# Kernel tuning notes

Measured on AMD Instinct MI355X. Metric: run time of the kernel, lower is better.

## Reference

```python
import jax, jax.numpy as jnp
import numpy as np

EPS = 1e-5


def setup_inputs() -> dict:
    key = jax.random.key(0)
    ks = jax.random.split(key, 10)
    B, C, H, W = 8, 128, 64, 64
    inputs = jax.random.normal(ks[0], (B, C, H, W), dtype=jnp.float32)
    # GroupNorm affine params
    gn_w = jnp.ones((C,), dtype=jnp.float32)
    gn_b = jnp.zeros((C,), dtype=jnp.float32)
    # Linear layers: torch nn.Linear weight is [out, in]
    s = 1.0 / np.sqrt(C)
    Wq = jax.random.uniform(ks[1], (C, C), jnp.float32, -s, s)
    bq = jax.random.uniform(ks[2], (C,), jnp.float32, -s, s)
    Wk = jax.random.uniform(ks[3], (C, C), jnp.float32, -s, s)
    bk = jax.random.uniform(ks[4], (C,), jnp.float32, -s, s)
    Wv = jax.random.uniform(ks[5], (C, C), jnp.float32, -s, s)
    bv = jax.random.uniform(ks[6], (C,), jnp.float32, -s, s)
    Wp = jax.random.uniform(ks[7], (C, C), jnp.float32, -s, s)
    bp = jax.random.uniform(ks[8], (C,), jnp.float32, -s, s)
    return {"inputs": inputs, "gn_w": gn_w, "gn_b": gn_b,
            "Wq": Wq, "bq": bq, "Wk": Wk, "bk": bk,
            "Wv": Wv, "bv": bv, "Wp": Wp, "bp": bp,
            "groups": 32}


def _group_norm(x, w, b, groups):
    B, C, H, W = x.shape
    xg = x.reshape(B, groups, C // groups, H, W)
    mu = jnp.mean(xg, axis=(2, 3, 4), keepdims=True)
    var = jnp.var(xg, axis=(2, 3, 4), keepdims=True)
    xn = ((xg - mu) * jax.lax.rsqrt(var + EPS)).reshape(B, C, H, W)
    return xn * w[None, :, None, None] + b[None, :, None, None]


def reference(inputs, gn_w, gn_b, Wq, bq, Wk, bk, Wv, bv, Wp, bp, groups):
    B, C, H, W = inputs.shape
    scale = C ** (-0.5)
    normed = _group_norm(inputs, gn_w, gn_b, groups)  # [B,C,H,W]
    x = normed.transpose(0, 2, 3, 1).reshape(B, H * W, C)  # [B,N,C] tokens
    q = x @ Wq.T + bq
    k = x @ Wk.T + bk
    v = x @ Wv.T + bv
    # full dense attention over N = H*W tokens, single head
    scores = jnp.einsum('bnc,bmc->bnm', q, k) * scale  # [B,N,N]
    attn = jax.nn.softmax(scores, axis=-1)
    out = jnp.einsum('bnm,bmc->bnc', attn, v)
    proj = out @ Wp.T + bp
    proj = proj.reshape(B, H, W, C).transpose(0, 3, 1, 2)
    return normed + proj
```

## Files before the change

### kernel.cpp

```cpp
#include <hip/hip_runtime.h>
#include <hip/hip_bf16.h>
#include <math.h>

typedef __bf16 bf16_t;
typedef __bf16 bf16x8 __attribute__((ext_vector_type(8)));
typedef float  f32x4  __attribute__((ext_vector_type(4)));
typedef float  f32x16 __attribute__((ext_vector_type(16)));

#define BB 8
#define CC 128
#define NN 4096
#define LDP 136
#define SCALE2 0.12751743342f

static __device__ __forceinline__ f32x4 mfma16(bf16x8 a, bf16x8 b, f32x4 c) {
    return __builtin_amdgcn_mfma_f32_16x16x32_bf16(a, b, c, 0, 0, 0);
}
static __device__ __forceinline__ f32x16 mfma32(bf16x8 a, bf16x8 b, f32x16 c) {
    return __builtin_amdgcn_mfma_f32_32x32x16_bf16(a, b, c, 0, 0, 0);
}
static __device__ __forceinline__ void gld16(const void* g, void* l) {
    __builtin_amdgcn_global_load_lds(
        (const __attribute__((address_space(1))) void*)g,
        (__attribute__((address_space(3))) void*)l, 16, 0, 0);
}
static __device__ __forceinline__ unsigned pack2bf(float a, float b) {
    union { bf16_t h[2]; unsigned u; } r;
    r.h[0] = (bf16_t)a; r.h[1] = (bf16_t)b;
    return r.u;
}

__global__ void __launch_bounds__(256) gn_stats(const float* __restrict__ in,
                                                float* __restrict__ stats) {
    int bg = blockIdx.x;
    const float4* p4 = (const float4*)(in + (size_t)bg * 16384);
    int tid = threadIdx.x;
    float s = 0.f, ss = 0.f;
    for (int i = tid; i < 4096; i += 256) {
        float4 v = p4[i];
        s  += v.x + v.y + v.z + v.w;
        ss += v.x*v.x + v.y*v.y + v.z*v.z + v.w*v.w;
    }
    for (int off = 1; off < 64; off <<= 1) {
        s  += __shfl_xor(s,  off, 64);
        ss += __shfl_xor(ss, off, 64);
    }
    __shared__ float red[8];
    int wv = tid >> 6;
    if ((tid & 63) == 0) { red[wv*2] = s; red[wv*2+1] = ss; }
    __syncthreads();
    if (tid == 0) {
        float S  = red[0]+red[2]+red[4]+red[6];
        float SS = red[1]+red[3]+red[5]+red[7];
        float mu  = S * (1.f/16384.f);
        float var = SS * (1.f/16384.f) - mu*mu;
        stats[bg*2]   = mu;
        stats[bg*2+1] = rsqrtf(var + 1e-5f);
    }
}

__global__ void __launch_bounds__(256) gn_apply(const float* __restrict__ in,
                                                const float* __restrict__ gw,
                                                const float* __restrict__ gb,
                                                const float* __restrict__ stats,
                                                bf16_t* __restrict__ x) {
    int b  = blockIdx.x >> 6;
    int p0 = (blockIdx.x & 63) << 6;
    int tid = threadIdx.x;
    __shared__ bf16_t tile[64 * 130];
    for (int i = tid; i < 8192; i += 256) {
        int c = i >> 6, p = i & 63;
        size_t idx = ((size_t)(b*CC + c)) * NN + p0 + p;
        float v = in[idx];
        int sg = b*32 + (c >> 2);
        float xn = (v - stats[sg*2]) * stats[sg*2+1] * gw[c] + gb[c];
        tile[p*130 + c] = (bf16_t)xn;
    }
    __syncthreads();
    bf16_t* xb = x + ((size_t)(b*NN + p0)) * CC;
    for (int i = tid; i < 4096; i += 256) {
        int p = i >> 6, cp = i & 63;
        unsigned int d = *(const unsigned int*)&tile[p*130 + cp*2];
        *(unsigned int*)&xb[p*CC + cp*2] = d;
    }
}

__global__ void __launch_bounds__(256) qkv_gemm(const bf16_t* __restrict__ x,
        const float* __restrict__ Wq, const float* __restrict__ bq,
        const float* __restrict__ Wk, const float* __restrict__ bk,
        const float* __restrict__ Wv, const float* __restrict__ bv,
        bf16_t* __restrict__ q, bf16_t* __restrict__ k, bf16_t* __restrict__ vT) {
    __shared__ bf16_t wb[CC * LDP];
    const int ph  = blockIdx.x >> 8;
    const int blk = blockIdx.x & 255;
    int b  = blk >> 5;
    int n0 = (blk & 31) << 7;
    int tid = threadIdx.x;
    int lane = tid & 63, l15 = lane & 15, quad = lane >> 4;
    int w = tid >> 6;
    bf16x8 afr[2][4];
    #pragma unroll
    for (int rt = 0; rt < 2; rt++)
        #pragma unroll
        for (int kb = 0; kb < 4; kb++)
            afr[rt][kb] = *(const bf16x8*)&x[(size_t)(b*NN + n0 + w*32 + rt*16 + l15)*CC + kb*32 + quad*8];

    const float* W  = (ph == 0) ? Wq : (ph == 1 ? Wk : Wv);
    const float* bs = (ph == 0) ? bq : (ph == 1 ? bk : bv);
    for (int i = tid; i < 2048; i += 256) {
        int row = i >> 4, s8 = i & 15;
        const float* wp = W + row*128 + s8*8;
        bf16x8 v;
        #pragma unroll
        for (int j = 0; j < 8; j++) v[j] = (bf16_t)wp[j];
        *(bf16x8*)&wb[row*LDP + s8*8] = v;
    }
    __syncthreads();
    f32x4 acc[2][8];
    f32x4 z = {0.f, 0.f, 0.f, 0.f};
    #pragma unroll
    for (int rt = 0; rt < 2; rt++)
        #pragma unroll
        for (int t = 0; t < 8; t++) acc[rt][t] = z;
    #pragma unroll
    for (int kb = 0; kb < 4; kb++)
        #pragma unroll
        for (int t = 0; t < 8; t++) {
            bf16x8 bf = *(const bf16x8*)&wb[(t*16 + l15)*LDP + kb*32 + quad*8];
            acc[0][t] = mfma16(afr[0][kb], bf, acc[0][t]);
            acc[1][t] = mfma16(afr[1][kb], bf, acc[1][t]);
        }
    __syncthreads();
    if (ph < 2) {
        float sc = (ph == 0) ? SCALE2 : 1.0f;
        #pragma unroll
        for (int t = 0; t < 8; t++) {
            float bias = bs[t*16 + l15];
            #pragma unroll
            for (int rt = 0; rt < 2; rt++)
                #pragma unroll
                for (int r = 0; r < 4; r++) {
                    int nloc = w*32 + rt*16 + quad*4 + r;
                    wb[nloc*LDP + t*16 + l15] = (bf16_t)((acc[rt][t][r] + bias) * sc);
                }
        }
        __syncthreads();
        bf16_t* outp = (ph == 0) ? q : k;
        for (int i = tid; i < 2048; i += 256) {
            int row = i >> 4, g = i & 15;
            bf16x8 vv = *(const bf16x8*)&wb[row*LDP + g*8];
            int gd = (ph == 0) ? g : (g ^ (row & 15));
            *(bf16x8*)&outp[(size_t)(b*NN + n0 + row)*CC + gd*8] = vv;
        }
    } else {
        #pragma unroll
        for (int t = 0; t < 8; t++) {
            float bias = bs[t*16 + l15];
            #pragma unroll
            for (int rt = 0; rt < 2; rt++)
                #pragma unroll
                for (int r = 0; r < 4; r++) {
                    int nloc = w*32 + rt*16 + quad*4 + r;
                    wb[(t*16 + l15)*LDP + nloc] = (bf16_t)(acc[rt][t][r] + bias);
                }
        }
        __syncthreads();
        for (int i = tid; i < 8192; i += 256) {
            int c = i >> 6, np = i & 63;
            unsigned int d = *(const unsigned int*)&wb[c*LDP + np*2];
            int npp = (np & ~6) | ((np & 2) << 1) | ((np & 4) >> 1);
            int g = (npp >> 2) ^ (c & 15);
            *(unsigned int*)&vT[(size_t)(b*CC + c)*NN + n0 + (g << 3) + ((npp & 3) << 1)] = d;
        }
    }
}

__global__ void __launch_bounds__(512, 2) flash_attn(const bf16_t* __restrict__ qg_,
                                                     const bf16_t* __restrict__ kg,
                                                     const bf16_t* __restrict__ vg,
                                                     unsigned* __restrict__ opd,
                                                     float* __restrict__ mlf) {
    __shared__ bf16_t kbuf[2][128*128];
    __shared__ bf16_t vbuf[2][128*128];
    const int b    = blockIdx.x >> 5;
    const int qb   = (blockIdx.x >> 1) & 15;
    const int jh   = blockIdx.x & 1;
    const int q0   = qb << 8;
    const int j00  = jh << 11;
    const int tid  = threadIdx.x;
    const int lane = tid & 63;
    const int l31  = lane & 31;
    const int h    = lane >> 5;
    const int w    = tid >> 6;

    bf16x8 qf[8];
    {
        const bf16_t* qr = qg_ + ((size_t)(b*NN + q0 + w*32 + l31))*CC + h*8;
        #pragma unroll
        for (int kc = 0; kc < 8; kc++) qf[kc] = *(const bf16x8*)(qr + kc*16);
    }
    int gofs[8];
    #pragma unroll
    for (int kc = 0; kc < 8; kc++) gofs[kc] = ((2*kc + h) ^ (l31 & 15)) << 3;

    f32x16 ot[4];
    #pragma unroll
    for (int ct = 0; ct < 4; ct++)
        #pragma unroll
        for (int r = 0; r < 16; r++) ot[ct][r] = 0.f;
    float l = 0.f;

    {
        const bf16_t* kt = kg + ((size_t)(b*NN + j00))*CC;
        #pragma unroll
        for (int it = 0; it < 4; it++) {
            int cb = it*512 + tid;
            gld16(kt + (size_t)cb*8, &kbuf[0][cb*8]);
        }
        #pragma unroll
        for (int it = 0; it < 4; it++) {
            int c = it*512 + tid;
            gld16(vg + ((size_t)(b*CC + (c >> 4)))*NN + j00 + (c & 15)*8, &vbuf[0][c*8]);
        }
    }
    __syncthreads();

    for (int i = 0; i < 16; i++) {
        const int cur = i & 1;
        if (i < 15) {
            const int j0n = j00 + ((i + 1) << 7);
            const bf16_t* kt = kg + ((size_t)(b*NN + j0n))*CC;
            #pragma unroll
            for (int it = 0; it < 4; it++) {
                int cb = it*512 + tid;
                gld16(kt + (size_t)cb*8, &kbuf[cur^1][cb*8]);
            }
            #pragma unroll
            for (int it = 0; it < 4; it++) {
                int c = it*512 + tid;
                gld16(vg + ((size_t)(b*CC + (c >> 4)))*NN + j0n + (c & 15)*8, &vbuf[cur^1][c*8]);
            }
        }
        f32x16 st[4];
        #pragma unroll
        for (int tt = 0; tt < 4; tt++)
            #pragma unroll
            for (int r = 0; r < 16; r++) st[tt][r] = 0.f;
        #pragma unroll
        for (int kc = 0; kc < 8; kc++) {
            #pragma unroll
            for (int tt = 0; tt < 4; tt++) {
                bf16x8 kf = *(const bf16x8*)&kbuf[cur][(tt*32 + l31)*128 + gofs[kc]];
                st[tt] = mfma32(kf, qf[kc], st[tt]);
            }
        }
        #pragma unroll
        for (int tt = 0; tt < 4; tt++) {
            #pragma unroll
            for (int r = 0; r < 16; r++) st[tt][r] = __builtin_amdgcn_exp2f(st[tt][r]);
            {
                float a0 = (st[tt][0]+st[tt][1]) + (st[tt][2]+st[tt][3]);
                float a1 = (st[tt][4]+st[tt][5]) + (st[tt][6]+st[tt][7]);
                float a2 = (st[tt][8]+st[tt][9]) + (st[tt][10]+st[tt][11]);
                float a3 = (st[tt][12]+st[tt][13]) + (st[tt][14]+st[tt][15]);
                l += (a0 + a1) + (a2 + a3);
            }
            union { unsigned u[4]; bf16x8 v; } pf[2];
            #pragma unroll
            for (int kcl = 0; kcl < 2; kcl++)
                #pragma unroll
                for (int g = 0; g < 4; g++)
                    pf[kcl].u[g] = pack2bf(st[tt][8*kcl + 2*g], st[tt][8*kcl + 2*g + 1]);
            #pragma unroll
            for (int kcl = 0; kcl < 2; kcl++) {
                const int kc = tt*2 + kcl;
                #pragma unroll
                for (int ct = 0; ct < 4; ct++) {
                    bf16x8 vf = *(const bf16x8*)&vbuf[cur][(ct*32 + l31)*128 + gofs[kc]];
                    ot[ct] = mfma32(vf, pf[kcl].v, ot[ct]);
                }
            }
        }
        __syncthreads();
    }
    l += __shfl_xor(l, 32, 64);
    const int row0 = q0 + w*32 + l31;
    unsigned* ob = opd + ((size_t)(jh*BB + b)) * 64 * NN;
    #pragma unroll
    for (int ct = 0; ct < 4; ct++)
        #pragma unroll
        for (int rp = 0; rp < 8; rp++) {
            int cpair = ct*16 + (rp & 1) + 4*(rp >> 1) + 2*h;
            ob[(size_t)cpair*NN + row0] = pack2bf(ot[ct][2*rp], ot[ct][2*rp + 1]);
        }
    if (h == 0)
        mlf[((size_t)(jh*BB + b))*NN + row0] = l;
}

__global__ void __launch_bounds__(256) merge_attn(const unsigned* __restrict__ opd,
                                                  const float* __restrict__ mlf,
                                                  bf16_t* __restrict__ ao) {
    __shared__ float inv[128];
    __shared__ unsigned tile[128 * 65];
    const int b  = blockIdx.x >> 5;
    const int q0 = (blockIdx.x & 31) << 7;
    const int tid = threadIdx.x;
    if (tid < 128) {
        float lt = 0.f;
        #pragma unroll
        for (int p = 0; p < 2; p++) lt += mlf[((size_t)(p*BB + b))*NN + q0 + tid];
        inv[tid] = 1.0f / lt;
    }
    __syncthreads();
    for (int i = tid; i < 8192; i += 256) {
        int q = i & 127, cp = i >> 7;
        float lo = 0.f, hi = 0.f;
        #pragma unroll
        for (int p = 0; p < 2; p++) {
            unsigned u = opd[(((size_t)(p*BB + b))*64 + cp)*NN + q0 + q];
            union { unsigned u; float f; } a, c;
            a.u = u << 16; c.u = u & 0xffff0000u;
            lo += a.f; hi += c.f;
        }
        float s = inv[q];
        tile[q*65 + cp] = pack2bf(lo * s, hi * s);
    }
    __syncthreads();
    unsigned* aod = (unsigned*)ao;
    for (int i = tid; i < 8192; i += 256) {
        int q = i >> 6, cp = i & 63;
        aod[((size_t)(b*NN + q0 + q))*64 + cp] = tile[q*65 + cp];
    }
}

__global__ void __launch_bounds__(256) proj_out(const bf16_t* __restrict__ ao,
                                                const float* __restrict__ Wp,
                                                const float* __restrict__ bp,
                                                const float* __restrict__ in,
                                                const float* __restrict__ stats,
                                                const float* __restrict__ gw,
                                                const float* __restrict__ gb,
                                                float* __restrict__ out) {
    __shared__ bf16_t wb[CC * LDP];
    int b  = blockIdx.x >> 5;
    int n0 = (blockIdx.x & 31) << 7;
    int tid = threadIdx.x;
    int lane = tid & 63, l15 = lane & 15, quad = lane >> 4;
    int w = tid >> 6;
    bf16x8 afr[2][4];
    #pragma unroll
    for (int rt = 0; rt < 2; rt++)
        #pragma unroll
        for (int kb = 0; kb < 4; kb++)
            afr[rt][kb] = *(const bf16x8*)&ao[(size_t)(b*NN + n0 + w*32 + rt*16 + l15)*CC + kb*32 + quad*8];
    for (int i = tid; i < 2048; i += 256) {
        int row = i >> 4, s8 = i & 15;
        const float* wp = Wp + row*128 + s8*8;
        bf16x8 v;
        #pragma unroll
        for (int j = 0; j < 8; j++) v[j] = (bf16_t)wp[j];
        *(bf16x8*)&wb[row*LDP + s8*8] = v;
    }
    __syncthreads();
    f32x4 acc[2][8];
    f32x4 z = {0.f, 0.f, 0.f, 0.f};
    #pragma unroll
    for (int rt = 0; rt < 2; rt++)
        #pragma unroll
        for (int t = 0; t < 8; t++) acc[rt][t] = z;
    #pragma unroll
    for (int kb = 0; kb < 4; kb++)
        #pragma unroll
        for (int t = 0; t < 8; t++) {
            bf16x8 bf = *(const bf16x8*)&wb[(t*16 + l15)*LDP + kb*32 + quad*8];
            acc[0][t] = mfma16(afr[0][kb], bf, acc[0][t]);
            acc[1][t] = mfma16(afr[1][kb], bf, acc[1][t]);
        }
    __syncthreads();
    #pragma unroll
    for (int t = 0; t < 8; t++) {
        float bias = bp[t*16 + l15];
        #pragma unroll
        for (int rt = 0; rt < 2; rt++)
            #pragma unroll
            for (int r = 0; r < 4; r++) {
                int nloc = w*32 + rt*16 + quad*4 + r;
                wb[(t*16 + l15)*LDP + nloc] = (bf16_t)(acc[rt][t][r] + bias);
            }
    }
    __syncthreads();
    for (int i = tid; i < 8192; i += 256) {
        int c = i >> 6, np = i & 63;
        bf16_t b0 = wb[c*LDP + np*2], b1 = wb[c*LDP + np*2 + 1];
        size_t idx = (size_t)(b*CC + c)*NN + n0 + np*2;
        int sg = b*32 + (c >> 2);
        float mu = stats[sg*2], rs = stats[sg*2+1];
        float gwc = gw[c], gbc = gb[c];
        float2 iv = *(const float2*)&in[idx];
        float2 ov;
        ov.x = (iv.x - mu)*rs*gwc + gbc + (float)b0;
        ov.y = (iv.y - mu)*rs*gwc + gbc + (float)b1;
        *(float2*)&out[idx] = ov;
    }
}

extern "C" void kernel_launch(void* const* d_in, const int* in_sizes, int n_in,
                              void* d_out, int out_size, void* d_ws, size_t ws_size,
                              hipStream_t stream) {
    const float* in = (const float*)d_in[0];
    const float* gw = (const float*)d_in[1];
    const float* gb = (const float*)d_in[2];
    const float* Wq = (const float*)d_in[3];
    const float* bq = (const float*)d_in[4];
    const float* Wk = (const float*)d_in[5];
    const float* bk = (const float*)d_in[6];
    const float* Wv = (const float*)d_in[7];
    const float* bv = (const float*)d_in[8];
    const float* Wp = (const float*)d_in[9];
    const float* bp = (const float*)d_in[10];
    float* out = (float*)d_out;

    char* ws = (char*)d_ws;
    const size_t SZ = (size_t)BB * NN * CC * 2;
    float*    stats = (float*)ws;
    bf16_t*   x  = (bf16_t*)(ws + 2048);
    bf16_t*   q  = (bf16_t*)(ws + 2048 + SZ);
    bf16_t*   kk = (bf16_t*)(ws + 2048 + 2*SZ);
    bf16_t*   vT = (bf16_t*)(ws + 2048 + 3*SZ);
    bf16_t*   ao = (bf16_t*)(ws + 2048 + 4*SZ);
    unsigned* op = (unsigned*)(ws + 2048 + 5*SZ);
    float*    ml = (float*)(ws + 2048 + 5*SZ + (size_t)2*BB*64*NN*4);

    gn_stats  <<<256, 256, 0, stream>>>(in, stats);
    gn_apply  <<<512, 256, 0, stream>>>(in, gw, gb, stats, x);
    qkv_gemm  <<<768, 256, 0, stream>>>(x, Wq, bq, Wk, bk, Wv, bv, q, kk, vT);
    flash_attn<<<256, 512, 0, stream>>>(q, kk, vT, op, ml);
    merge_attn<<<256, 256, 0, stream>>>(op, ml, ao);
    proj_out  <<<256, 256, 0, stream>>>(ao, Wp, bp, in, stats, gw, gb, out);
}
```

Measured before the change: 203.1 us.

## Fuse GroupNorm apply into QKV GEMM and attention merge into output projection

The separate gn_apply kernel is folded into qkv_gemm. Each block now normalizes its 128-token slab into LDS and computes Q, K and V in a loop over three phases, reloading the weight tile between phases. The merge_attn kernel is folded into proj_out, which combines the two split-KV partial outputs and normalizes them into LDS before the projection GEMM. This removes two launches and the global round trips of the normalized x and merged attention output. In exchange the QKV grid shrinks from 768 to 256 blocks and LDS use per block roughly doubles, which may reduce occupancy and parallelism.

```diff
diff --git a/kernel.cpp b/kernel.cpp
--- a/kernel.cpp
+++ b/kernel.cpp
@@ -59,118 +59,119 @@
     }
 }
 
-__global__ void __launch_bounds__(256) gn_apply(const float* __restrict__ in,
-                                                const float* __restrict__ gw,
-                                                const float* __restrict__ gb,
-                                                const float* __restrict__ stats,
-                                                bf16_t* __restrict__ x) {
-    int b  = blockIdx.x >> 6;
-    int p0 = (blockIdx.x & 63) << 6;
-    int tid = threadIdx.x;
-    __shared__ bf16_t tile[64 * 130];
-    for (int i = tid; i < 8192; i += 256) {
-        int c = i >> 6, p = i & 63;
-        size_t idx = ((size_t)(b*CC + c)) * NN + p0 + p;
-        float v = in[idx];
-        int sg = b*32 + (c >> 2);
-        float xn = (v - stats[sg*2]) * stats[sg*2+1] * gw[c] + gb[c];
-        tile[p*130 + c] = (bf16_t)xn;
-    }
-    __syncthreads();
-    bf16_t* xb = x + ((size_t)(b*NN + p0)) * CC;
-    for (int i = tid; i < 4096; i += 256) {
-        int p = i >> 6, cp = i & 63;
-        unsigned int d = *(const unsigned int*)&tile[p*130 + cp*2];
-        *(unsigned int*)&xb[p*CC + cp*2] = d;
-    }
-}
-
-__global__ void __launch_bounds__(256) qkv_gemm(const bf16_t* __restrict__ x,
+__global__ void __launch_bounds__(256) qkv_gemm(const float* __restrict__ in,
+        const float* __restrict__ stats, const float* __restrict__ gw, const float* __restrict__ gb,
         const float* __restrict__ Wq, const float* __restrict__ bq,
         const float* __restrict__ Wk, const float* __restrict__ bk,
         const float* __restrict__ Wv, const float* __restrict__ bv,
         bf16_t* __restrict__ q, bf16_t* __restrict__ k, bf16_t* __restrict__ vT) {
     __shared__ bf16_t wb[CC * LDP];
-    const int ph  = blockIdx.x >> 8;
-    const int blk = blockIdx.x & 255;
-    int b  = blk >> 5;
-    int n0 = (blk & 31) << 7;
+    __shared__ bf16_t xt[128 * 130];
+    int b  = blockIdx.x >> 5;
+    int n0 = (blockIdx.x & 31) << 7;
     int tid = threadIdx.x;
     int lane = tid & 63, l15 = lane & 15, quad = lane >> 4;
     int w = tid >> 6;
-    bf16x8 afr[2][4];
-    #pragma unroll
-    for (int rt = 0; rt < 2; rt++)
-        #pragma unroll
-        for (int kb = 0; kb < 4; kb++)
-            afr[rt][kb] = *(const bf16x8*)&x[(size_t)(b*NN + n0 + w*32 + rt*16 + l15)*CC + kb*32 + quad*8];
-
-    const float* W  = (ph == 0) ? Wq : (ph == 1 ? Wk : Wv);
-    const float* bs = (ph == 0) ? bq : (ph == 1 ? bk : bv);
+
+    for (int i = tid; i < 4096; i += 256) {
+        int c = i >> 5, p4 = i & 31;
+        const float4* inp = (const float4*)(in + (size_t)(b*CC + c)*NN + n0);
+        float4 v = inp[p4];
+        int sg = b*32 + (c >> 2);
+        float mu = stats[sg*2], rs = stats[sg*2+1];
+        float gwc = gw[c], gbc = gb[c];
+        xt[(p4*4 + 0)*130 + c] = (bf16_t)((v.x - mu)*rs*gwc + gbc);
+        xt[(p4*4 + 1)*130 + c] = (bf16_t)((v.y - mu)*rs*gwc + gbc);
+        xt[(p4*4 + 2)*130 + c] = (bf16_t)((v.z - mu)*rs*gwc + gbc);
+        xt[(p4*4 + 3)*130 + c] = (bf16_t)((v.w - mu)*rs*gwc + gbc);
+    }
     for (int i = tid; i < 2048; i += 256) {
         int row = i >> 4, s8 = i & 15;
-        const float* wp = W + row*128 + s8*8;
+        const float* wp = Wq + row*128 + s8*8;
         bf16x8 v;
         #pragma unroll
         for (int j = 0; j < 8; j++) v[j] = (bf16_t)wp[j];
         *(bf16x8*)&wb[row*LDP + s8*8] = v;
     }
     __syncthreads();
-    f32x4 acc[2][8];
-    f32x4 z = {0.f, 0.f, 0.f, 0.f};
+    bf16x8 afr[2][4];
     #pragma unroll
     for (int rt = 0; rt < 2; rt++)
         #pragma unroll
-        for (int t = 0; t < 8; t++) acc[rt][t] = z;
-    #pragma unroll
-    for (int kb = 0; kb < 4; kb++)
-        #pragma unroll
-        for (int t = 0; t < 8; t++) {
-            bf16x8 bf = *(const bf16x8*)&wb[(t*16 + l15)*LDP + kb*32 + quad*8];
-            acc[0][t] = mfma16(afr[0][kb], bf, acc[0][t]);
-            acc[1][t] = mfma16(afr[1][kb], bf, acc[1][t]);
-        }
-    __syncthreads();
-    if (ph < 2) {
-        float sc = (ph == 0) ? SCALE2 : 1.0f;
-        #pragma unroll
-        for (int t = 0; t < 8; t++) {
-            float bias = bs[t*16 + l15];
-            #pragma unroll
-            for (int rt = 0; rt < 2; rt++)
+        for (int kb = 0; kb < 4; kb++)
+            afr[rt][kb] = *(const bf16x8*)&xt[(w*32 + rt*16 + l15)*130 + kb*32 + quad*8];
+
+    for (int ph = 0; ph < 3; ph++) {
+        const float* bs = (ph == 0) ? bq : (ph == 1 ? bk : bv);
+        f32x4 acc[2][8];
+        f32x4 z = {0.f, 0.f, 0.f, 0.f};
+        #pragma unroll
+        for (int rt = 0; rt < 2; rt++)
+            #pragma unroll
+            for (int t = 0; t < 8; t++) acc[rt][t] = z;
+        #pragma unroll
+        for (int kb = 0; kb < 4; kb++)
+            #pragma unroll
+            for (int t = 0; t < 8; t++) {
+                bf16x8 bf = *(const bf16x8*)&wb[(t*16 + l15)*LDP + kb*32 + quad*8];
+                acc[0][t] = mfma16(afr[0][kb], bf, acc[0][t]);
+                acc[1][t] = mfma16(afr[1][kb], bf, acc[1][t]);
+            }
+        __syncthreads();
+        if (ph < 2) {
+            float sc = (ph == 0) ? SCALE2 : 1.0f;
+            #pragma unroll
+            for (int t = 0; t < 8; t++) {
+                float bias = bs[t*16 + l15];
                 #pragma unroll
-                for (int r = 0; r < 4; r++) {
-                    int nloc = w*32 + rt*16 + quad*4 + r;
-                    wb[nloc*LDP + t*16 + l15] = (bf16_t)((acc[rt][t][r] + bias) * sc);
-                }
-        }
-        __syncthreads();
-        bf16_t* outp = (ph == 0) ? q : k;
-        for (int i = tid; i < 2048; i += 256) {
-            int row = i >> 4, g = i & 15;
-            bf16x8 vv = *(const bf16x8*)&wb[row*LDP + g*8];
-            int gd = (ph == 0) ? g : (g ^ (row & 15));
-            *(bf16x8*)&outp[(size_t)(b*NN + n0 + row)*CC + gd*8] = vv;
-        }
-    } else {
-        #pragma unroll
-        for (int t = 0; t < 8; t++) {
-            float bias = bs[t*16 + l15];
-            #pragma unroll
-            for (int rt = 0; rt < 2; rt++)
+                for (int rt = 0; rt < 2; rt++)
+                    #pragma unroll
+                    for (int r = 0; r < 4; r++) {
+                        int nloc = w*32 + rt*16 + quad*4 + r;
+                        wb[nloc*LDP + t*16 + l15] = (bf16_t)((acc[rt][t][r] + bias) * sc);
+                    }
+            }
+            __syncthreads();
+            bf16_t* outp = (ph == 0) ? q : k;
+            for (int i = tid; i < 2048; i += 256) {
+                int row = i >> 4, g = i & 15;
+                bf16x8 vv = *(const bf16x8*)&wb[row*LDP + g*8];
+                int gd = (ph == 0) ? g : (g ^ (row & 15));
+                *(bf16x8*)&outp[(size_t)(b*NN + n0 + row)*CC + gd*8] = vv;
+            }
+        } else {
+            #pragma unroll
+            for (int t = 0; t < 8; t++) {
+                float bias = bs[t*16 + l15];
                 #pragma unroll
-                for (int r = 0; r < 4; r++) {
-                    int nloc = w*32 + rt*16 + quad*4 + r;
-                    wb[(t*16 + l15)*LDP + nloc] = (bf16_t)(acc[rt][t][r] + bias);
-                }
-        }
-        __syncthreads();
-        for (int i = tid; i < 8192; i += 256) {
-            int c = i >> 6, np = i & 63;
-            unsigned int d = *(const unsigned int*)&wb[c*LDP + np*2];
-            int npp = (np & ~6) | ((np & 2) << 1) | ((np & 4) >> 1);
-            int g = (npp >> 2) ^ (c & 15);
-            *(unsigned int*)&vT[(size_t)(b*CC + c)*NN + n0 + (g << 3) + ((npp & 3) << 1)] = d;
+                for (int rt = 0; rt < 2; rt++)
+                    #pragma unroll
+                    for (int r = 0; r < 4; r++) {
+                        int nloc = w*32 + rt*16 + quad*4 + r;
+                        wb[(t*16 + l15)*LDP + nloc] = (bf16_t)(acc[rt][t][r] + bias);
+                    }
+            }
+            __syncthreads();
+            for (int i = tid; i < 8192; i += 256) {
+                int c = i >> 6, np = i & 63;
+                unsigned int d = *(const unsigned int*)&wb[c*LDP + np*2];
+                int npp = (np & ~6) | ((np & 2) << 1) | ((np & 4) >> 1);
+                int g = (npp >> 2) ^ (c & 15);
+                *(unsigned int*)&vT[(size_t)(b*CC + c)*NN + n0 + (g << 3) + ((npp & 3) << 1)] = d;
+            }
+        }
+        if (ph < 2) {
+            __syncthreads();
+            const float* Wn = (ph == 0) ? Wk : Wv;
+            for (int i = tid; i < 2048; i += 256) {
+                int row = i >> 4, s8 = i & 15;
+                const float* wp = Wn + row*128 + s8*8;
+                bf16x8 v;
+                #pragma unroll
+                for (int j = 0; j < 8; j++) v[j] = (bf16_t)wp[j];
+                *(bf16x8*)&wb[row*LDP + s8*8] = v;
+            }
+            __syncthreads();
         }
     }
 }
@@ -297,43 +298,8 @@
         mlf[((size_t)(jh*BB + b))*NN + row0] = l;
 }
 
-__global__ void __launch_bounds__(256) merge_attn(const unsigned* __restrict__ opd,
-                                                  const float* __restrict__ mlf,
-                                                  bf16_t* __restrict__ ao) {
-    __shared__ float inv[128];
-    __shared__ unsigned tile[128 * 65];
-    const int b  = blockIdx.x >> 5;
-    const int q0 = (blockIdx.x & 31) << 7;
-    const int tid = threadIdx.x;
-    if (tid < 128) {
-        float lt = 0.f;
-        #pragma unroll
-        for (int p = 0; p < 2; p++) lt += mlf[((size_t)(p*BB + b))*NN + q0 + tid];
-        inv[tid] = 1.0f / lt;
-    }
-    __syncthreads();
-    for (int i = tid; i < 8192; i += 256) {
-        int q = i & 127, cp = i >> 7;
-        float lo = 0.f, hi = 0.f;
-        #pragma unroll
-        for (int p = 0; p < 2; p++) {
-            unsigned u = opd[(((size_t)(p*BB + b))*64 + cp)*NN + q0 + q];
-            union { unsigned u; float f; } a, c;
-            a.u = u << 16; c.u = u & 0xffff0000u;
-            lo += a.f; hi += c.f;
-        }
-        float s = inv[q];
-        tile[q*65 + cp] = pack2bf(lo * s, hi * s);
-    }
-    __syncthreads();
-    unsigned* aod = (unsigned*)ao;
-    for (int i = tid; i < 8192; i += 256) {
-        int q = i >> 6, cp = i & 63;
-        aod[((size_t)(b*NN + q0 + q))*64 + cp] = tile[q*65 + cp];
-    }
-}
-
-__global__ void __launch_bounds__(256) proj_out(const bf16_t* __restrict__ ao,
+__global__ void __launch_bounds__(256) proj_out(const unsigned* __restrict__ opd,
+                                                const float* __restrict__ mlf,
                                                 const float* __restrict__ Wp,
                                                 const float* __restrict__ bp,
                                                 const float* __restrict__ in,
@@ -342,17 +308,17 @@
                                                 const float* __restrict__ gb,
                                                 float* __restrict__ out) {
     __shared__ bf16_t wb[CC * LDP];
+    __shared__ bf16_t aot[128 * 130];
+    __shared__ float invl[128];
     int b  = blockIdx.x >> 5;
     int n0 = (blockIdx.x & 31) << 7;
     int tid = threadIdx.x;
     int lane = tid & 63, l15 = lane & 15, quad = lane >> 4;
     int w = tid >> 6;
-    bf16x8 afr[2][4];
-    #pragma unroll
-    for (int rt = 0; rt < 2; rt++)
-        #pragma unroll
-        for (int kb = 0; kb < 4; kb++)
-            afr[rt][kb] = *(const bf16x8*)&ao[(size_t)(b*NN + n0 + w*32 + rt*16 + l15)*CC + kb*32 + quad*8];
+    if (tid < 128) {
+        float lt = mlf[(size_t)b*NN + n0 + tid] + mlf[((size_t)(BB + b))*NN + n0 + tid];
+        invl[tid] = 1.0f / lt;
+    }
     for (int i = tid; i < 2048; i += 256) {
         int row = i >> 4, s8 = i & 15;
         const float* wp = Wp + row*128 + s8*8;
@@ -362,6 +328,26 @@
         *(bf16x8*)&wb[row*LDP + s8*8] = v;
     }
     __syncthreads();
+    for (int i = tid; i < 8192; i += 256) {
+        int qq = i & 127, cp = i >> 7;
+        float lo = 0.f, hi = 0.f;
+        #pragma unroll
+        for (int p = 0; p < 2; p++) {
+            unsigned u = opd[(((size_t)(p*BB + b))*64 + cp)*NN + n0 + qq];
+            union { unsigned u; float f; } a, c;
+            a.u = u << 16; c.u = u & 0xffff0000u;
+            lo += a.f; hi += c.f;
+        }
+        float s = invl[qq];
+        *(unsigned*)&aot[qq*130 + cp*2] = pack2bf(lo * s, hi * s);
+    }
+    __syncthreads();
+    bf16x8 afr[2][4];
+    #pragma unroll
+    for (int rt = 0; rt < 2; rt++)
+        #pragma unroll
+        for (int kb = 0; kb < 4; kb++)
+            afr[rt][kb] = *(const bf16x8*)&aot[(w*32 + rt*16 + l15)*130 + kb*32 + quad*8];
     f32x4 acc[2][8];
     f32x4 z = {0.f, 0.f, 0.f, 0.f};
     #pragma unroll
@@ -423,18 +409,14 @@
     char* ws = (char*)d_ws;
     const size_t SZ = (size_t)BB * NN * CC * 2;
     float*    stats = (float*)ws;
-    bf16_t*   x  = (bf16_t*)(ws + 2048);
-    bf16_t*   q  = (bf16_t*)(ws + 2048 + SZ);
-    bf16_t*   kk = (bf16_t*)(ws + 2048 + 2*SZ);
-    bf16_t*   vT = (bf16_t*)(ws + 2048 + 3*SZ);
-    bf16_t*   ao = (bf16_t*)(ws + 2048 + 4*SZ);
-    unsigned* op = (unsigned*)(ws + 2048 + 5*SZ);
-    float*    ml = (float*)(ws + 2048 + 5*SZ + (size_t)2*BB*64*NN*4);
+    bf16_t*   q  = (bf16_t*)(ws + 2048);
+    bf16_t*   kk = (bf16_t*)(ws + 2048 + SZ);
+    bf16_t*   vT = (bf16_t*)(ws + 2048 + 2*SZ);
+    unsigned* op = (unsigned*)(ws + 2048 + 3*SZ);
+    float*    ml = (float*)(ws + 2048 + 3*SZ + (size_t)2*BB*64*NN*4);
 
     gn_stats  <<<256, 256, 0, stream>>>(in, stats);
-    gn_apply  <<<512, 256, 0, stream>>>(in, gw, gb, stats, x);
-    qkv_gemm  <<<768, 256, 0, stream>>>(x, Wq, bq, Wk, bk, Wv, bv, q, kk, vT);
+    qkv_gemm  <<<256, 256, 0, stream>>>(in, stats, gw, gb, Wq, bq, Wk, bk, Wv, bv, q, kk, vT);
     flash_attn<<<256, 512, 0, stream>>>(q, kk, vT, op, ml);
-    merge_attn<<<256, 256, 0, stream>>>(op, ml, ao);
-    proj_out  <<<256, 256, 0, stream>>>(ao, Wp, bp, in, stats, gw, gb, out);
-}
+    proj_out  <<<256, 256, 0, stream>>>(op, ml, Wp, bp, in, stats, gw, gb, out);
+}
```

Measured after the change: 191.9 us. 5.5% less time.
